# Performance work log

Measured on AMD Instinct MI355X. Metric: run time of the kernel, lower is better.

The kernel has to match this reference:

```python
import jax, jax.numpy as jnp
import numpy as np

EPS = 1e-10

def conv1x1(x, W, b):
    # x:[B,C,H,W], W:[O,C], b:[O]
    return jnp.einsum('bchw,oc->bohw', x, W) + b[None, :, None, None]

def setup_inputs() -> dict:
    key = jax.random.key(0)
    ks = jax.random.split(key, 16)
    B, C, H, W = 8, 512, 32, 32
    R, heads = 4, 8
    s = 1.0 / np.sqrt(C)
    inp = {
        'x': jax.random.normal(ks[0], (B, C, H, W), jnp.float32),
        'u_q': jax.random.uniform(ks[1], (B, R, H, W), jnp.float32, minval=EPS, maxval=1.0),
        'u_k': jax.random.uniform(ks[2], (B, R, H, W), jnp.float32, minval=EPS, maxval=1.0),
        'wq_s': jax.random.normal(ks[3], (R, C), jnp.float32) * s,
        'bq_s': jnp.zeros((R,), jnp.float32),
        'wk_s': jax.random.normal(ks[4], (R, C), jnp.float32) * s,
        'bk_s': jnp.zeros((R,), jnp.float32),
        'Wq': jax.random.normal(ks[5], (C, C), jnp.float32) * s,
        'bq': jnp.zeros((C,), jnp.float32),
        'Wk': jax.random.normal(ks[6], (C, C), jnp.float32) * s,
        'bk': jnp.zeros((C,), jnp.float32),
        'Wv': jax.random.normal(ks[7], (C, C), jnp.float32) * s,
        'bv': jnp.zeros((C,), jnp.float32),
        'Wp': jax.random.normal(ks[8], (C, C), jnp.float32) * s,
        'bp': jnp.zeros((C,), jnp.float32),
    }
    return inp

def reference(x, u_q, u_k, wq_s, bq_s, wk_s, bk_s, Wq, bq, Wk, bk, Wv, bv, Wp, bp):
    B, C, H, W = x.shape
    heads = 8
    hd = C // heads
    scale = hd ** -0.5
    N = H * W

    # gumbel-softmax hard=True then take channel 0 == (argmax(logits+g, dim=1) == 0)
    def sel_mask(ws, bs, u):
        logits = conv1x1(x, ws, bs)                       # [B,R,H,W]
        g = -jnp.log(-jnp.log(u + EPS) + EPS)             # gumbel noise
        m = jnp.argmax(logits + g, axis=1) == 0           # [B,H,W] bool
        return m.reshape(B, N)

    mq = jax.lax.stop_gradient(sel_mask(wq_s, bq_s, u_q))  # selected query points
    mk = jax.lax.stop_gradient(sel_mask(wk_s, bk_s, u_k))  # selected key/value points

    q = conv1x1(x, Wq, bq).reshape(B, heads, hd, N)
    k = conv1x1(x, Wk, bk).reshape(B, heads, hd, N)
    v = conv1x1(x, Wv, bv).reshape(B, heads, hd, N)

    # attention restricted to selected key positions (softmax over masked set
    # == softmax over the gathered subset in the torch code)
    attn = jnp.einsum('bhdn,bhdm->bhnm', q * scale, k)     # [B,h,N,N]
    attn = jnp.where(mk[:, None, None, :], attn, -1e30)
    attn = jax.nn.softmax(attn, axis=-1)
    out = jnp.einsum('bhnm,bhdm->bhdn', attn, v)           # [B,h,hd,N]

    # scatter attention output back into v at the selected query positions
    v_new = jnp.where(mq[:, None, :], out.reshape(B, C, N), v.reshape(B, C, N))
    v_new = v_new.reshape(B, C, H, W)
    return conv1x1(v_new, Wp, bp)
```

## Files before the change

kernel.cpp:

```cpp
#include <hip/hip_runtime.h>
#include <hip/hip_bf16.h>

#define B_ 8
#define C_ 512
#define N_ 1024
#define HEADS_ 8
#define HD_ 64

using f32x4  = __attribute__((ext_vector_type(4))) float;
using bf16x8 = __attribute__((ext_vector_type(8))) __bf16;

__device__ __forceinline__ unsigned short f2bf(float f) {
  union { float f; unsigned u; } v; v.f = f;
  unsigned r = v.u + 0x7FFFu + ((v.u >> 16) & 1u);
  return (unsigned short)(r >> 16);
}

__device__ __forceinline__ void gload16(const void* g, void* l) {
  __builtin_amdgcn_global_load_lds(
      (const __attribute__((address_space(1))) unsigned int*)g,
      (__attribute__((address_space(3))) unsigned int*)l, 16, 0, 0);
}

__global__ __launch_bounds__(256) void k_convw(
    const float* __restrict__ wq, const float* __restrict__ wk,
    const float* __restrict__ wv, const float* __restrict__ wp,
    unsigned short* __restrict__ out) {
  int i = blockIdx.x * 256 + threadIdx.x;
  int mat = i >> 16, idx4 = i & 65535;
  const float* src = (mat == 0) ? wq : (mat == 1) ? wk : (mat == 2) ? wv : wp;
  float4 v = ((const float4*)src)[idx4];
  unsigned lo = (unsigned)f2bf(v.x) | ((unsigned)f2bf(v.y) << 16);
  unsigned hi = (unsigned)f2bf(v.z) | ((unsigned)f2bf(v.w) << 16);
  uint2 u; u.x = lo; u.y = hi;
  ((uint2*)out)[i] = u;
}

__global__ __launch_bounds__(256) void k_transpose_x(
    const float* __restrict__ x, unsigned short* __restrict__ xT) {
  __shared__ float tile[64][65];
  int n0 = blockIdx.x * 64, c0 = blockIdx.y * 64, b = blockIdx.z;
  int t = threadIdx.x, tr = t >> 2, tc = (t & 3) * 16;
  const float* src = x + ((size_t)b * C_ + c0) * N_ + n0;
#pragma unroll
  for (int i = 0; i < 4; i++) {
    float4 v4 = *(const float4*)(src + (size_t)tr * N_ + tc + i * 4);
    tile[tr][tc + i * 4 + 0] = v4.x; tile[tr][tc + i * 4 + 1] = v4.y;
    tile[tr][tc + i * 4 + 2] = v4.z; tile[tr][tc + i * 4 + 3] = v4.w;
  }
  __syncthreads();
  unsigned short* dst = xT + ((size_t)b * N_ + n0) * C_ + c0;
#pragma unroll
  for (int i = 0; i < 4; i++) {
    unsigned short o4[4];
#pragma unroll
    for (int j = 0; j < 4; j++) o4[j] = f2bf(tile[tc + i * 4 + j][tr]);
    unsigned lo = (unsigned)o4[0] | ((unsigned)o4[1] << 16);
    unsigned hi = (unsigned)o4[2] | ((unsigned)o4[3] << 16);
    uint2 u; u.x = lo; u.y = hi;
    *(uint2*)(dst + (size_t)tr * C_ + tc + i * 4) = u;
  }
}

__global__ __launch_bounds__(256) void k_mask(
    const float* __restrict__ x, const float* __restrict__ u_q, const float* __restrict__ u_k,
    const float* __restrict__ wqs, const float* __restrict__ bqs,
    const float* __restrict__ wks, const float* __restrict__ bks,
    unsigned int* __restrict__ sel) {
  __shared__ float wq_l[4][512];
  __shared__ float wk_l[4][512];
  __shared__ float part[8 * 32 * 9];
  int b = blockIdx.y;
  int n0 = blockIdx.x * 32;
  int t = threadIdx.x, nl = t & 31, ch = t >> 5;
  for (int i = t; i < 2048; i += 256) {
    wq_l[i >> 9][i & 511] = wqs[i];
    wk_l[i >> 9][i & 511] = wks[i];
  }
  __syncthreads();
  int cbase = ch * 64;
  const float* xp = x + ((size_t)b * C_ + cbase) * N_ + n0 + nl;
  float sq[4] = {0.f, 0.f, 0.f, 0.f};
  float sk[4] = {0.f, 0.f, 0.f, 0.f};
  for (int c = 0; c < 64; c++) {
    float xv = xp[(size_t)c * N_];
#pragma unroll
    for (int r = 0; r < 4; r++) {
      sq[r] = fmaf(wq_l[r][cbase + c], xv, sq[r]);
      sk[r] = fmaf(wk_l[r][cbase + c], xv, sk[r]);
    }
  }
  float* pp = part + (ch * 32 + nl) * 9;
#pragma unroll
  for (int r = 0; r < 4; r++) { pp[r] = sq[r]; pp[4 + r] = sk[r]; }
  __syncthreads();
  if (t < 32) {
    int n = n0 + t;
    float fq[4], fk[4];
#pragma unroll
    for (int r = 0; r < 4; r++) { fq[r] = bqs[r]; fk[r] = bks[r]; }
#pragma unroll
    for (int c2 = 0; c2 < 8; c2++) {
      const float* q2 = part + (c2 * 32 + t) * 9;
#pragma unroll
      for (int r = 0; r < 4; r++) { fq[r] += q2[r]; fk[r] += q2[4 + r]; }
    }
#pragma unroll
    for (int r = 0; r < 4; r++) {
      float uq = u_q[((size_t)b * 4 + r) * N_ + n];
      float uk = u_k[((size_t)b * 4 + r) * N_ + n];
      fq[r] += -logf(-logf(uq + 1e-10f) + 1e-10f);
      fk[r] += -logf(-logf(uk + 1e-10f) + 1e-10f);
    }
    bool selq = (fq[0] >= fq[1]) && (fq[0] >= fq[2]) && (fq[0] >= fq[3]);
    bool selk = (fk[0] >= fk[1]) && (fk[0] >= fk[2]) && (fk[0] >= fk[3]);
    sel[(size_t)b * N_ + n] = selq ? 1u : 0u;
    sel[(size_t)(B_ + b) * N_ + n] = selk ? 1u : 0u;
  }
}

__global__ __launch_bounds__(1024) void k_scan(
    const unsigned int* __restrict__ sel, unsigned int* __restrict__ idx,
    unsigned int* __restrict__ cnt) {
  int which = blockIdx.x, b = blockIdx.y;
  const unsigned int* s = sel + ((size_t)which * B_ + b) * N_;
  unsigned int* ip = idx + ((size_t)which * B_ + b) * N_;
  int t = threadIdx.x, lane = t & 63, w = t >> 6;
  __shared__ unsigned int wtot[16], woff[16], totsh;
  unsigned int f = s[t];
  unsigned long long bal = __ballot(f != 0);
  unsigned int wpre = __popcll(bal & ((1ull << lane) - 1ull));
  if (lane == 0) wtot[w] = (unsigned int)__popcll(bal);
  __syncthreads();
  if (t == 0) {
    unsigned int acc = 0;
#pragma unroll
    for (int i = 0; i < 16; i++) { woff[i] = acc; acc += wtot[i]; }
    totsh = acc;
    cnt[which * B_ + b] = acc;
  }
  __syncthreads();
  unsigned int tot = totsh;
  if (f) ip[woff[w] + wpre] = (unsigned int)t;
  if (t >= (int)tot) ip[t] = 0u;
}

template <int MODE>
__global__ __launch_bounds__(256) void k_gemm(
    const unsigned short* __restrict__ Wall, const unsigned short* __restrict__ Bt,
    const float* __restrict__ bias0, const float* __restrict__ bias1,
    const float* __restrict__ bias2,
    const unsigned int* __restrict__ idx, const unsigned int* __restrict__ cnt,
    void* __restrict__ outv) {
  __shared__ __align__(16) unsigned short a_lds[2][128 * 64];
  __shared__ __align__(16) unsigned short b_lds[2][128 * 64];
  int z = blockIdx.z;
  int mat = (MODE == 0) ? (z >> 3) : 0;
  int b   = (MODE == 0) ? (z & 7) : z;
  int n0 = blockIdx.x * 128;
  if (MODE == 0 && mat < 2 && n0 >= (int)cnt[mat * B_ + b]) return;
  const unsigned short* A = Wall + (size_t)mat * 262144;
  const float* bias = (mat == 0) ? bias0 : (mat == 1) ? bias1 : bias2;
  int m0 = blockIdx.y * 128;
  int t = threadIdx.x, wave = t >> 6, lane = t & 63;
  int wr = (wave >> 1) * 64, wc = (wave & 1) * 64;
  f32x4 acc[4][4] = {};
  int srow = t >> 3, spch = t & 7;
  int lch = spch ^ (srow & 7);
  const unsigned short* aptr[4];
  const unsigned short* bptr[4];
#pragma unroll
  for (int i = 0; i < 4; i++) {
    int row = srow + i * 32;
    aptr[i] = A + (size_t)(m0 + row) * C_ + lch * 8;
    int grow = n0 + row;
    int srcr = (MODE == 0 && mat < 2) ? (int)idx[((size_t)mat * B_ + b) * N_ + grow] : grow;
    bptr[i] = Bt + ((size_t)b * N_ + srcr) * C_ + lch * 8;
  }
#define STAGE_(buf, kt) do { int k0_ = (kt) * 64;                                   \
    _Pragma("unroll") for (int i_ = 0; i_ < 4; i_++) {                              \
      gload16(aptr[i_] + k0_, (char*)a_lds + (buf) * 16384 + wave * 1024 + i_ * 4096); \
      gload16(bptr[i_] + k0_, (char*)b_lds + (buf) * 16384 + wave * 1024 + i_ * 4096); \
    } } while (0)
  STAGE_(0, 0);
  for (int kt = 0; kt < 8; kt++) {
    int cur = kt & 1;
    if (kt < 7) {
      STAGE_(cur ^ 1, kt + 1);
      asm volatile("s_waitcnt vmcnt(8)" ::: "memory");
    } else {
      asm volatile("s_waitcnt vmcnt(0)" ::: "memory");
    }
    __builtin_amdgcn_s_barrier();
    const unsigned short* al = a_lds[cur];
    const unsigned short* bl = b_lds[cur];
#pragma unroll
    for (int ks = 0; ks < 2; ks++) {
      bf16x8 af[4], bfr[4];
#pragma unroll
      for (int mi = 0; mi < 4; mi++) {
        int row = wr + mi * 16 + (lane & 15);
        int pch = (ks * 4 + (lane >> 4)) ^ (row & 7);
        af[mi] = *(const bf16x8*)(al + row * 64 + pch * 8);
      }
#pragma unroll
      for (int ni = 0; ni < 4; ni++) {
        int row = wc + ni * 16 + (lane & 15);
        int pch = (ks * 4 + (lane >> 4)) ^ (row & 7);
        bfr[ni] = *(const bf16x8*)(bl + row * 64 + pch * 8);
      }
#pragma unroll
      for (int mi = 0; mi < 4; mi++)
#pragma unroll
        for (int ni = 0; ni < 4; ni++)
          acc[mi][ni] = __builtin_amdgcn_mfma_f32_16x16x32_bf16(af[mi], bfr[ni], acc[mi][ni], 0, 0, 0);
    }
    __builtin_amdgcn_s_barrier();
  }
#undef STAGE_
  if (MODE == 0) {
    unsigned short* outp = (unsigned short*)outv + (size_t)mat * B_ * N_ * C_ + (size_t)b * N_ * C_;
#pragma unroll
    for (int mi = 0; mi < 4; mi++) {
      int ob = m0 + wr + mi * 16 + ((lane >> 4) << 2);
      float bs[4];
#pragma unroll
      for (int r = 0; r < 4; r++) bs[r] = bias[ob + r];
#pragma unroll
      for (int ni = 0; ni < 4; ni++) {
        int n = n0 + wc + ni * 16 + (lane & 15);
        unsigned short o4[4];
#pragma unroll
        for (int r = 0; r < 4; r++) o4[r] = f2bf(acc[mi][ni][r] + bs[r]);
        unsigned lo = (unsigned)o4[0] | ((unsigned)o4[1] << 16);
        unsigned hi = (unsigned)o4[2] | ((unsigned)o4[3] << 16);
        uint2 u; u.x = lo; u.y = hi;
        *(uint2*)(outp + (size_t)n * C_ + ob) = u;
      }
    }
  } else {
    float* outp = (float*)outv + (size_t)b * C_ * N_;
#pragma unroll
    for (int mi = 0; mi < 4; mi++) {
      int ob = m0 + wr + mi * 16 + ((lane >> 4) << 2);
#pragma unroll
      for (int r = 0; r < 4; r++) {
        float bv = bias[ob + r];
#pragma unroll
        for (int ni = 0; ni < 4; ni++) {
          int n = n0 + wc + ni * 16 + (lane & 15);
          outp[(size_t)(ob + r) * N_ + n] = acc[mi][ni][r] + bv;
        }
      }
    }
  }
}

__global__ __launch_bounds__(256) void k_gather_vt(
    const unsigned short* __restrict__ vT, const unsigned int* __restrict__ idx,
    const unsigned int* __restrict__ cnt, unsigned short* __restrict__ vctr) {
  int b = blockIdx.z;
  unsigned int nk = cnt[B_ + b];
  int j0 = blockIdx.x * 64;
  if (j0 >= (int)nk) return;
  int c0 = blockIdx.y * 64;
  __shared__ unsigned short tile[64][72];
  int t = threadIdx.x, tr = t >> 2, tc = (t & 3) * 16;
  int jj = j0 + tr;
  bool valid = jj < (int)nk;
  unsigned int srow = valid ? idx[((size_t)B_ + b) * N_ + jj] : 0u;
  const unsigned short* src = vT + ((size_t)b * N_ + srow) * C_ + c0;
#pragma unroll
  for (int i = 0; i < 4; i++) {
    ushort4 v4 = {0, 0, 0, 0};
    if (valid) v4 = *(const ushort4*)(src + tc + i * 4);
    tile[tr][tc + i * 4 + 0] = v4.x; tile[tr][tc + i * 4 + 1] = v4.y;
    tile[tr][tc + i * 4 + 2] = v4.z; tile[tr][tc + i * 4 + 3] = v4.w;
  }
  __syncthreads();
  unsigned short* dst = vctr + ((size_t)b * C_ + c0) * N_ + j0;
#pragma unroll
  for (int i = 0; i < 4; i++) {
    unsigned short o4[4];
#pragma unroll
    for (int j = 0; j < 4; j++) o4[j] = tile[tc + i * 4 + j][tr];
    unsigned lo = (unsigned)o4[0] | ((unsigned)o4[1] << 16);
    unsigned hi = (unsigned)o4[2] | ((unsigned)o4[3] << 16);
    uint2 u; u.x = lo; u.y = hi;
    *(uint2*)(dst + (size_t)tr * N_ + tc + i * 4) = u;
  }
}

__global__ __launch_bounds__(256) void k_attn(
    const unsigned short* __restrict__ qc, const unsigned short* __restrict__ kc,
    const unsigned short* __restrict__ vctr, unsigned short* __restrict__ vnew,
    const unsigned int* __restrict__ idx, const unsigned int* __restrict__ cnt) {
  __shared__ __align__(16) unsigned short p_lds[4][16 * 72];
  __shared__ float macc[4][16][65];
  __shared__ float mml[4][2][16];
  int qt = blockIdx.x, h = blockIdx.y, b = blockIdx.z;
  int nq = (int)cnt[b], nk = (int)cnt[B_ + b];
  int q0 = qt * 16;
  if (q0 >= nq) return;
  int t = threadIdx.x, wave = t >> 6, lane = t & 63;
  const unsigned short* qp =
      qc + ((size_t)b * N_ + q0 + (lane & 15)) * C_ + h * HD_ + ((lane >> 4) * 8);
  bf16x8 qf0 = *(const bf16x8*)qp;
  bf16x8 qf1 = *(const bf16x8*)(qp + 32);
  float mrow[4], lrow[4];
  f32x4 acc[4];
#pragma unroll
  for (int r = 0; r < 4; r++) { mrow[r] = -1e30f; lrow[r] = 0.f; }
#pragma unroll
  for (int d = 0; d < 4; d++) acc[d] = f32x4{0.f, 0.f, 0.f, 0.f};
  for (int j0 = wave * 64; j0 < nk; j0 += 256) {
    f32x4 s[4];
#pragma unroll
    for (int nf = 0; nf < 4; nf++) {
      const unsigned short* kp =
          kc + ((size_t)b * N_ + j0 + nf * 16 + (lane & 15)) * C_ + h * HD_ + ((lane >> 4) * 8);
      bf16x8 kf0 = *(const bf16x8*)kp;
      bf16x8 kf1 = *(const bf16x8*)(kp + 32);
      f32x4 z = {0.f, 0.f, 0.f, 0.f};
      z = __builtin_amdgcn_mfma_f32_16x16x32_bf16(qf0, kf0, z, 0, 0, 0);
      z = __builtin_amdgcn_mfma_f32_16x16x32_bf16(qf1, kf1, z, 0, 0, 0);
      float mv = ((j0 + nf * 16 + (lane & 15)) < nk) ? 0.f : -1e30f;
#pragma unroll
      for (int r = 0; r < 4; r++) s[nf][r] = z[r] * 0.125f + mv;
    }
    float alpha[4];
#pragma unroll
    for (int r = 0; r < 4; r++) {
      float mx = fmaxf(fmaxf(s[0][r], s[1][r]), fmaxf(s[2][r], s[3][r]));
      mx = fmaxf(mx, __shfl_xor(mx, 1));
      mx = fmaxf(mx, __shfl_xor(mx, 2));
      mx = fmaxf(mx, __shfl_xor(mx, 4));
      mx = fmaxf(mx, __shfl_xor(mx, 8));
      float mn = fmaxf(mrow[r], mx);
      alpha[r] = __expf(mrow[r] - mn);
      mrow[r] = mn;
      float rs = 0.f;
      int ql = ((lane >> 4) << 2) + r;
#pragma unroll
      for (int nf = 0; nf < 4; nf++) {
        float sv = s[nf][r];
        float p = (sv < -1e29f) ? 0.f : __expf(sv - mn);
        rs += p;
        p_lds[wave][ql * 72 + nf * 16 + (lane & 15)] = f2bf(p);
      }
      rs += __shfl_xor(rs, 1);
      rs += __shfl_xor(rs, 2);
      rs += __shfl_xor(rs, 4);
      rs += __shfl_xor(rs, 8);
      lrow[r] = lrow[r] * alpha[r] + rs;
    }
    bf16x8 pa0 = *(const bf16x8*)&p_lds[wave][(lane & 15) * 72 + ((lane >> 4) * 8)];
    bf16x8 pa1 = *(const bf16x8*)&p_lds[wave][(lane & 15) * 72 + 32 + ((lane >> 4) * 8)];
#pragma unroll
    for (int df = 0; df < 4; df++) {
#pragma unroll
      for (int r = 0; r < 4; r++) acc[df][r] *= alpha[r];
      const unsigned short* vp =
          vctr + ((size_t)b * C_ + h * HD_ + df * 16 + (lane & 15)) * N_ + j0 + ((lane >> 4) * 8);
      bf16x8 vf0 = *(const bf16x8*)vp;
      bf16x8 vf1 = *(const bf16x8*)(vp + 32);
      acc[df] = __builtin_amdgcn_mfma_f32_16x16x32_bf16(pa0, vf0, acc[df], 0, 0, 0);
      acc[df] = __builtin_amdgcn_mfma_f32_16x16x32_bf16(pa1, vf1, acc[df], 0, 0, 0);
    }
  }
#pragma unroll
  for (int df = 0; df < 4; df++)
#pragma unroll
    for (int r = 0; r < 4; r++)
      macc[wave][((lane >> 4) << 2) + r][df * 16 + (lane & 15)] = acc[df][r];
  if ((lane & 15) == 0) {
#pragma unroll
    for (int r = 0; r < 4; r++) {
      mml[wave][0][((lane >> 4) << 2) + r] = mrow[r];
      mml[wave][1][((lane >> 4) << 2) + r] = lrow[r];
    }
  }
  __syncthreads();
  {
    int q = t >> 4, d0 = (t & 15) * 4;
    float mg = fmaxf(fmaxf(mml[0][0][q], mml[1][0][q]), fmaxf(mml[2][0][q], mml[3][0][q]));
    float lg = 0.f, o0 = 0.f, o1 = 0.f, o2 = 0.f, o3 = 0.f;
#pragma unroll
    for (int w = 0; w < 4; w++) {
      float sc = __expf(mml[w][0][q] - mg);
      lg += mml[w][1][q] * sc;
      o0 += macc[w][q][d0 + 0] * sc;
      o1 += macc[w][q][d0 + 1] * sc;
      o2 += macc[w][q][d0 + 2] * sc;
      o3 += macc[w][q][d0 + 3] * sc;
    }
    if (q0 + q < nq) {
      unsigned int qrow = idx[(size_t)b * N_ + q0 + q];
      float inv = 1.0f / lg;
      unsigned short o4[4] = {f2bf(o0 * inv), f2bf(o1 * inv), f2bf(o2 * inv), f2bf(o3 * inv)};
      unsigned lo = (unsigned)o4[0] | ((unsigned)o4[1] << 16);
      unsigned hi = (unsigned)o4[2] | ((unsigned)o4[3] << 16);
      uint2 u; u.x = lo; u.y = hi;
      *(uint2*)(vnew + ((size_t)b * N_ + qrow) * C_ + h * HD_ + d0) = u;
    }
  }
}

extern "C" void kernel_launch(void* const* d_in, const int* in_sizes, int n_in,
                              void* d_out, int out_size, void* d_ws, size_t ws_size,
                              hipStream_t stream) {
  const float* x   = (const float*)d_in[0];
  const float* u_q = (const float*)d_in[1];
  const float* u_k = (const float*)d_in[2];
  const float* wqs = (const float*)d_in[3];
  const float* bqs = (const float*)d_in[4];
  const float* wks = (const float*)d_in[5];
  const float* bks = (const float*)d_in[6];
  const float* Wq  = (const float*)d_in[7];
  const float* bq  = (const float*)d_in[8];
  const float* Wk  = (const float*)d_in[9];
  const float* bk  = (const float*)d_in[10];
  const float* Wv  = (const float*)d_in[11];
  const float* bv  = (const float*)d_in[12];
  const float* Wp  = (const float*)d_in[13];
  const float* bp  = (const float*)d_in[14];

  char* ws = (char*)d_ws;
  unsigned short* xT   = (unsigned short*)(ws);
  unsigned short* wbf  = (unsigned short*)(ws + 8388608);
  unsigned short* qkv  = (unsigned short*)(ws + 10485760);
  unsigned short* qc   = qkv;
  unsigned short* kc   = qkv + (size_t)B_ * N_ * C_;
  unsigned short* vT   = kc + (size_t)B_ * N_ * C_;
  unsigned short* vctr = (unsigned short*)(ws + 35651584);
  unsigned int*   sel  = (unsigned int*)(ws + 44040192);
  unsigned int*   idx  = (unsigned int*)(ws + 44105728);
  unsigned int*   cnt  = (unsigned int*)(ws + 44171264);

  k_convw<<<dim3(1024), 256, 0, stream>>>(Wq, Wk, Wv, Wp, wbf);
  k_transpose_x<<<dim3(16, 8, 8), 256, 0, stream>>>(x, xT);
  k_mask<<<dim3(32, 8), 256, 0, stream>>>(x, u_q, u_k, wqs, bqs, wks, bks, sel);
  k_scan<<<dim3(2, 8), 1024, 0, stream>>>(sel, idx, cnt);
  k_gemm<0><<<dim3(8, 4, 24), 256, 0, stream>>>(wbf, xT, bq, bk, bv, idx, cnt, (void*)qkv);
  k_gather_vt<<<dim3(16, 8, 8), 256, 0, stream>>>(vT, idx, cnt, vctr);
  k_attn<<<dim3(64, 8, 8), 256, 0, stream>>>(qc, kc, vctr, vT, idx, cnt);
  k_gemm<1><<<dim3(8, 4, 8), 256, 0, stream>>>(wbf + 3 * 262144, vT, bp, bp, bp, idx, cnt, d_out);
}
```

Baseline: 167.7 us.

## Merge prep kernels into one launch and halve GEMM N-tile to 64

The weight conversion, x transpose and mask kernels are merged into a single k_prep launch that dispatches on block id ranges, removing two kernel launches and their serialization gaps. The projection GEMMs switch from 128x128 to 128x64 tiles, doubling the grid size for better CU occupancy on the 256-CU device, and cut per-block LDS and accumulator registers. The smaller tile lowers data reuse per block and raises total A-matrix traffic.

```diff
diff --git a/kernel.cpp b/kernel.cpp
--- a/kernel.cpp
+++ b/kernel.cpp
@@ -22,100 +22,101 @@
       (__attribute__((address_space(3))) unsigned int*)l, 16, 0, 0);
 }
 
-__global__ __launch_bounds__(256) void k_convw(
-    const float* __restrict__ wq, const float* __restrict__ wk,
-    const float* __restrict__ wv, const float* __restrict__ wp,
-    unsigned short* __restrict__ out) {
-  int i = blockIdx.x * 256 + threadIdx.x;
-  int mat = i >> 16, idx4 = i & 65535;
-  const float* src = (mat == 0) ? wq : (mat == 1) ? wk : (mat == 2) ? wv : wp;
-  float4 v = ((const float4*)src)[idx4];
-  unsigned lo = (unsigned)f2bf(v.x) | ((unsigned)f2bf(v.y) << 16);
-  unsigned hi = (unsigned)f2bf(v.z) | ((unsigned)f2bf(v.w) << 16);
-  uint2 u; u.x = lo; u.y = hi;
-  ((uint2*)out)[i] = u;
-}
-
-__global__ __launch_bounds__(256) void k_transpose_x(
-    const float* __restrict__ x, unsigned short* __restrict__ xT) {
-  __shared__ float tile[64][65];
-  int n0 = blockIdx.x * 64, c0 = blockIdx.y * 64, b = blockIdx.z;
-  int t = threadIdx.x, tr = t >> 2, tc = (t & 3) * 16;
-  const float* src = x + ((size_t)b * C_ + c0) * N_ + n0;
-#pragma unroll
-  for (int i = 0; i < 4; i++) {
-    float4 v4 = *(const float4*)(src + (size_t)tr * N_ + tc + i * 4);
-    tile[tr][tc + i * 4 + 0] = v4.x; tile[tr][tc + i * 4 + 1] = v4.y;
-    tile[tr][tc + i * 4 + 2] = v4.z; tile[tr][tc + i * 4 + 3] = v4.w;
-  }
-  __syncthreads();
-  unsigned short* dst = xT + ((size_t)b * N_ + n0) * C_ + c0;
-#pragma unroll
-  for (int i = 0; i < 4; i++) {
-    unsigned short o4[4];
-#pragma unroll
-    for (int j = 0; j < 4; j++) o4[j] = f2bf(tile[tc + i * 4 + j][tr]);
-    unsigned lo = (unsigned)o4[0] | ((unsigned)o4[1] << 16);
-    unsigned hi = (unsigned)o4[2] | ((unsigned)o4[3] << 16);
-    uint2 u; u.x = lo; u.y = hi;
-    *(uint2*)(dst + (size_t)tr * C_ + tc + i * 4) = u;
-  }
-}
-
-__global__ __launch_bounds__(256) void k_mask(
+__global__ __launch_bounds__(256) void k_prep(
     const float* __restrict__ x, const float* __restrict__ u_q, const float* __restrict__ u_k,
     const float* __restrict__ wqs, const float* __restrict__ bqs,
     const float* __restrict__ wks, const float* __restrict__ bks,
+    const float* __restrict__ Wq, const float* __restrict__ Wk,
+    const float* __restrict__ Wv, const float* __restrict__ Wp,
+    unsigned short* __restrict__ xT, unsigned short* __restrict__ wbf,
     unsigned int* __restrict__ sel) {
-  __shared__ float wq_l[4][512];
-  __shared__ float wk_l[4][512];
-  __shared__ float part[8 * 32 * 9];
-  int b = blockIdx.y;
-  int n0 = blockIdx.x * 32;
-  int t = threadIdx.x, nl = t & 31, ch = t >> 5;
-  for (int i = t; i < 2048; i += 256) {
-    wq_l[i >> 9][i & 511] = wqs[i];
-    wk_l[i >> 9][i & 511] = wks[i];
-  }
-  __syncthreads();
-  int cbase = ch * 64;
-  const float* xp = x + ((size_t)b * C_ + cbase) * N_ + n0 + nl;
-  float sq[4] = {0.f, 0.f, 0.f, 0.f};
-  float sk[4] = {0.f, 0.f, 0.f, 0.f};
-  for (int c = 0; c < 64; c++) {
-    float xv = xp[(size_t)c * N_];
-#pragma unroll
-    for (int r = 0; r < 4; r++) {
-      sq[r] = fmaf(wq_l[r][cbase + c], xv, sq[r]);
-      sk[r] = fmaf(wk_l[r][cbase + c], xv, sk[r]);
-    }
-  }
-  float* pp = part + (ch * 32 + nl) * 9;
-#pragma unroll
-  for (int r = 0; r < 4; r++) { pp[r] = sq[r]; pp[4 + r] = sk[r]; }
-  __syncthreads();
-  if (t < 32) {
-    int n = n0 + t;
-    float fq[4], fk[4];
-#pragma unroll
-    for (int r = 0; r < 4; r++) { fq[r] = bqs[r]; fk[r] = bks[r]; }
-#pragma unroll
-    for (int c2 = 0; c2 < 8; c2++) {
-      const float* q2 = part + (c2 * 32 + t) * 9;
-#pragma unroll
-      for (int r = 0; r < 4; r++) { fq[r] += q2[r]; fk[r] += q2[4 + r]; }
-    }
-#pragma unroll
-    for (int r = 0; r < 4; r++) {
-      float uq = u_q[((size_t)b * 4 + r) * N_ + n];
-      float uk = u_k[((size_t)b * 4 + r) * N_ + n];
-      fq[r] += -logf(-logf(uq + 1e-10f) + 1e-10f);
-      fk[r] += -logf(-logf(uk + 1e-10f) + 1e-10f);
-    }
-    bool selq = (fq[0] >= fq[1]) && (fq[0] >= fq[2]) && (fq[0] >= fq[3]);
-    bool selk = (fk[0] >= fk[1]) && (fk[0] >= fk[2]) && (fk[0] >= fk[3]);
-    sel[(size_t)b * N_ + n] = selq ? 1u : 0u;
-    sel[(size_t)(B_ + b) * N_ + n] = selk ? 1u : 0u;
+  __shared__ __align__(16) char smem[25600];
+  int id = blockIdx.x;
+  int t = threadIdx.x;
+  if (id < 256) {
+    float* wq_l = (float*)smem;
+    float* wk_l = wq_l + 2048;
+    float* part = wk_l + 2048;
+    int b = id >> 5;
+    int n0 = (id & 31) * 32;
+    int nl = t & 31, ch = t >> 5;
+    for (int i = t; i < 2048; i += 256) {
+      wq_l[i] = wqs[i];
+      wk_l[i] = wks[i];
+    }
+    __syncthreads();
+    int cbase = ch * 64;
+    const float* xp = x + ((size_t)b * C_ + cbase) * N_ + n0 + nl;
+    float sq[4] = {0.f, 0.f, 0.f, 0.f};
+    float sk[4] = {0.f, 0.f, 0.f, 0.f};
+    for (int c = 0; c < 64; c++) {
+      float xv = xp[(size_t)c * N_];
+#pragma unroll
+      for (int r = 0; r < 4; r++) {
+        sq[r] = fmaf(wq_l[r * 512 + cbase + c], xv, sq[r]);
+        sk[r] = fmaf(wk_l[r * 512 + cbase + c], xv, sk[r]);
+      }
+    }
+    float* pp = part + (ch * 32 + nl) * 9;
+#pragma unroll
+    for (int r = 0; r < 4; r++) { pp[r] = sq[r]; pp[4 + r] = sk[r]; }
+    __syncthreads();
+    if (t < 32) {
+      int n = n0 + t;
+      float fq[4], fk[4];
+#pragma unroll
+      for (int r = 0; r < 4; r++) { fq[r] = bqs[r]; fk[r] = bks[r]; }
+#pragma unroll
+      for (int c2 = 0; c2 < 8; c2++) {
+        const float* q2 = part + (c2 * 32 + t) * 9;
+#pragma unroll
+        for (int r = 0; r < 4; r++) { fq[r] += q2[r]; fk[r] += q2[4 + r]; }
+      }
+#pragma unroll
+      for (int r = 0; r < 4; r++) {
+        float uq = u_q[((size_t)b * 4 + r) * N_ + n];
+        float uk = u_k[((size_t)b * 4 + r) * N_ + n];
+        fq[r] += -logf(-logf(uq + 1e-10f) + 1e-10f);
+        fk[r] += -logf(-logf(uk + 1e-10f) + 1e-10f);
+      }
+      bool selq = (fq[0] >= fq[1]) && (fq[0] >= fq[2]) && (fq[0] >= fq[3]);
+      bool selk = (fk[0] >= fk[1]) && (fk[0] >= fk[2]) && (fk[0] >= fk[3]);
+      sel[(size_t)b * N_ + n] = selq ? 1u : 0u;
+      sel[(size_t)(B_ + b) * N_ + n] = selk ? 1u : 0u;
+    }
+  } else if (id < 1280) {
+    float (*tile)[65] = (float(*)[65])smem;
+    int m = id - 256;
+    int n0 = (m & 15) * 64, c0 = ((m >> 4) & 7) * 64, b = m >> 7;
+    int tr = t >> 2, tc = (t & 3) * 16;
+    const float* src = x + ((size_t)b * C_ + c0) * N_ + n0;
+#pragma unroll
+    for (int i = 0; i < 4; i++) {
+      float4 v4 = *(const float4*)(src + (size_t)tr * N_ + tc + i * 4);
+      tile[tr][tc + i * 4 + 0] = v4.x; tile[tr][tc + i * 4 + 1] = v4.y;
+      tile[tr][tc + i * 4 + 2] = v4.z; tile[tr][tc + i * 4 + 3] = v4.w;
+    }
+    __syncthreads();
+    unsigned short* dst = xT + ((size_t)b * N_ + n0) * C_ + c0;
+#pragma unroll
+    for (int i = 0; i < 4; i++) {
+      unsigned short o4[4];
+#pragma unroll
+      for (int j = 0; j < 4; j++) o4[j] = f2bf(tile[tc + i * 4 + j][tr]);
+      unsigned lo = (unsigned)o4[0] | ((unsigned)o4[1] << 16);
+      unsigned hi = (unsigned)o4[2] | ((unsigned)o4[3] << 16);
+      uint2 u; u.x = lo; u.y = hi;
+      *(uint2*)(dst + (size_t)tr * C_ + tc + i * 4) = u;
+    }
+  } else {
+    int i = (id - 1280) * 256 + t;
+    int mat = i >> 16, idx4 = i & 65535;
+    const float* src = (mat == 0) ? Wq : (mat == 1) ? Wk : (mat == 2) ? Wv : Wp;
+    float4 v = ((const float4*)src)[idx4];
+    unsigned lo = (unsigned)f2bf(v.x) | ((unsigned)f2bf(v.y) << 16);
+    unsigned hi = (unsigned)f2bf(v.z) | ((unsigned)f2bf(v.w) << 16);
+    uint2 u; u.x = lo; u.y = hi;
+    ((uint2*)wbf)[i] = u;
   }
 }
 
@@ -153,41 +154,43 @@
     const unsigned int* __restrict__ idx, const unsigned int* __restrict__ cnt,
     void* __restrict__ outv) {
   __shared__ __align__(16) unsigned short a_lds[2][128 * 64];
-  __shared__ __align__(16) unsigned short b_lds[2][128 * 64];
+  __shared__ __align__(16) unsigned short b_lds[2][64 * 64];
   int z = blockIdx.z;
   int mat = (MODE == 0) ? (z >> 3) : 0;
   int b   = (MODE == 0) ? (z & 7) : z;
-  int n0 = blockIdx.x * 128;
+  int n0 = blockIdx.x * 64;
   if (MODE == 0 && mat < 2 && n0 >= (int)cnt[mat * B_ + b]) return;
   const unsigned short* A = Wall + (size_t)mat * 262144;
   const float* bias = (mat == 0) ? bias0 : (mat == 1) ? bias1 : bias2;
   int m0 = blockIdx.y * 128;
   int t = threadIdx.x, wave = t >> 6, lane = t & 63;
-  int wr = (wave >> 1) * 64, wc = (wave & 1) * 64;
-  f32x4 acc[4][4] = {};
+  int wr = (wave >> 1) * 64, wc = (wave & 1) * 32;
+  f32x4 acc[4][2] = {};
   int srow = t >> 3, spch = t & 7;
   int lch = spch ^ (srow & 7);
   const unsigned short* aptr[4];
-  const unsigned short* bptr[4];
-#pragma unroll
-  for (int i = 0; i < 4; i++) {
-    int row = srow + i * 32;
-    aptr[i] = A + (size_t)(m0 + row) * C_ + lch * 8;
-    int grow = n0 + row;
+  const unsigned short* bptr[2];
+#pragma unroll
+  for (int i = 0; i < 4; i++)
+    aptr[i] = A + (size_t)(m0 + srow + i * 32) * C_ + lch * 8;
+#pragma unroll
+  for (int i = 0; i < 2; i++) {
+    int grow = n0 + srow + i * 32;
     int srcr = (MODE == 0 && mat < 2) ? (int)idx[((size_t)mat * B_ + b) * N_ + grow] : grow;
     bptr[i] = Bt + ((size_t)b * N_ + srcr) * C_ + lch * 8;
   }
-#define STAGE_(buf, kt) do { int k0_ = (kt) * 64;                                   \
-    _Pragma("unroll") for (int i_ = 0; i_ < 4; i_++) {                              \
-      gload16(aptr[i_] + k0_, (char*)a_lds + (buf) * 16384 + wave * 1024 + i_ * 4096); \
-      gload16(bptr[i_] + k0_, (char*)b_lds + (buf) * 16384 + wave * 1024 + i_ * 4096); \
-    } } while (0)
+#define STAGE_(buf, kt) do { int k0_ = (kt) * 64;                                          \
+    _Pragma("unroll") for (int i_ = 0; i_ < 4; i_++)                                       \
+      gload16(aptr[i_] + k0_, (char*)a_lds + (buf) * 16384 + wave * 1024 + i_ * 4096);     \
+    _Pragma("unroll") for (int i_ = 0; i_ < 2; i_++)                                       \
+      gload16(bptr[i_] + k0_, (char*)b_lds + (buf) * 8192 + wave * 1024 + i_ * 4096);      \
+    } while (0)
   STAGE_(0, 0);
   for (int kt = 0; kt < 8; kt++) {
     int cur = kt & 1;
     if (kt < 7) {
       STAGE_(cur ^ 1, kt + 1);
-      asm volatile("s_waitcnt vmcnt(8)" ::: "memory");
+      asm volatile("s_waitcnt vmcnt(6)" ::: "memory");
     } else {
       asm volatile("s_waitcnt vmcnt(0)" ::: "memory");
     }
@@ -196,7 +199,7 @@
     const unsigned short* bl = b_lds[cur];
 #pragma unroll
     for (int ks = 0; ks < 2; ks++) {
-      bf16x8 af[4], bfr[4];
+      bf16x8 af[4], bfr[2];
 #pragma unroll
       for (int mi = 0; mi < 4; mi++) {
         int row = wr + mi * 16 + (lane & 15);
@@ -204,7 +207,7 @@
         af[mi] = *(const bf16x8*)(al + row * 64 + pch * 8);
       }
 #pragma unroll
-      for (int ni = 0; ni < 4; ni++) {
+      for (int ni = 0; ni < 2; ni++) {
         int row = wc + ni * 16 + (lane & 15);
         int pch = (ks * 4 + (lane >> 4)) ^ (row & 7);
         bfr[ni] = *(const bf16x8*)(bl + row * 64 + pch * 8);
@@ -212,7 +215,7 @@
 #pragma unroll
       for (int mi = 0; mi < 4; mi++)
 #pragma unroll
-        for (int ni = 0; ni < 4; ni++)
+        for (int ni = 0; ni < 2; ni++)
           acc[mi][ni] = __builtin_amdgcn_mfma_f32_16x16x32_bf16(af[mi], bfr[ni], acc[mi][ni], 0, 0, 0);
     }
     __builtin_amdgcn_s_barrier();
@@ -227,7 +230,7 @@
 #pragma unroll
       for (int r = 0; r < 4; r++) bs[r] = bias[ob + r];
 #pragma unroll
-      for (int ni = 0; ni < 4; ni++) {
+      for (int ni = 0; ni < 2; ni++) {
         int n = n0 + wc + ni * 16 + (lane & 15);
         unsigned short o4[4];
 #pragma unroll
@@ -247,7 +250,7 @@
       for (int r = 0; r < 4; r++) {
         float bv = bias[ob + r];
 #pragma unroll
-        for (int ni = 0; ni < 4; ni++) {
+        for (int ni = 0; ni < 2; ni++) {
           int n = n0 + wc + ni * 16 + (lane & 15);
           outp[(size_t)(ob + r) * N_ + n] = acc[mi][ni][r] + bv;
         }
@@ -437,12 +440,11 @@
   unsigned int*   idx  = (unsigned int*)(ws + 44105728);
   unsigned int*   cnt  = (unsigned int*)(ws + 44171264);
 
-  k_convw<<<dim3(1024), 256, 0, stream>>>(Wq, Wk, Wv, Wp, wbf);
-  k_transpose_x<<<dim3(16, 8, 8), 256, 0, stream>>>(x, xT);
-  k_mask<<<dim3(32, 8), 256, 0, stream>>>(x, u_q, u_k, wqs, bqs, wks, bks, sel);
+  k_prep<<<dim3(2304), 256, 0, stream>>>(x, u_q, u_k, wqs, bqs, wks, bks,
+                                         Wq, Wk, Wv, Wp, xT, wbf, sel);
   k_scan<<<dim3(2, 8), 1024, 0, stream>>>(sel, idx, cnt);
-  k_gemm<0><<<dim3(8, 4, 24), 256, 0, stream>>>(wbf, xT, bq, bk, bv, idx, cnt, (void*)qkv);
+  k_gemm<0><<<dim3(16, 4, 24), 256, 0, stream>>>(wbf, xT, bq, bk, bv, idx, cnt, (void*)qkv);
   k_gather_vt<<<dim3(16, 8, 8), 256, 0, stream>>>(vT, idx, cnt, vctr);
   k_attn<<<dim3(64, 8, 8), 256, 0, stream>>>(qc, kc, vctr, vT, idx, cnt);
-  k_gemm<1><<<dim3(8, 4, 8), 256, 0, stream>>>(wbf + 3 * 262144, vT, bp, bp, bp, idx, cnt, d_out);
-}
+  k_gemm<1><<<dim3(16, 4, 8), 256, 0, stream>>>(wbf + 3 * 262144, vT, bp, bp, bp, idx, cnt, d_out);
+}
```

Result: no change. 164.5 us (-1.9%).
